# Performance work log

Hardware: AMD Instinct MI355X
Metric: run time of the kernel (lower is better)

Reference implementation:

```python
import jax, jax.numpy as jnp
import numpy as np

B, C, HID, H, W = 32, 256, 128, 32, 32  # batch, input_dim, hidden_dim, grid


def conv1x1(x, Wt, b):
    # 1x1 Conv2d == channel-mixing matmul. x: [B,Cin,H,W], Wt: [Cout,Cin]
    return jnp.einsum('oc,bchw->bohw', Wt, x) + b[None, :, None, None]


def setup_inputs() -> dict:
    key = jax.random.key(0)
    ks = jax.random.split(key, 18)
    p = lambda k, shape: (jax.random.normal(k, shape, jnp.float32) * 0.02)
    return {
        'h': jax.random.normal(ks[0], (B, C, H, W), jnp.float32),
        'm': jax.random.normal(ks[1], (B, C, H, W), jnp.float32),
        'Wq': p(ks[2], (HID, C)),  'bq': p(ks[3], (HID,)),
        'Wk': p(ks[4], (HID, C)),  'bk': p(ks[5], (HID,)),
        'Wv': p(ks[6], (C, C)),    'bv': p(ks[7], (C,)),
        'Wk2': p(ks[8], (HID, C)), 'bk2': p(ks[9], (HID,)),
        'Wv2': p(ks[10], (C, C)),  'bv2': p(ks[11], (C,)),
        'Wz': p(ks[12], (2 * C, 2 * C)), 'bz': p(ks[13], (2 * C,)),
        'Wm': p(ks[14], (3 * C, 3 * C)), 'bm': p(ks[15], (3 * C,)),
    }


def reference(h, m, Wq, bq, Wk, bk, Wv, bv, Wk2, bk2, Wv2, bv2, Wz, bz, Wm, bm):
    Bb, Cc, Hh, Ww = h.shape
    HW = Hh * Ww
    # shared query from h: [B, HID, HW]
    q = conv1x1(h, Wq, bq).reshape(Bb, -1, HW)
    # self-attention branch over h (unscaled logits, as in original)
    kh = conv1x1(h, Wk, bk).reshape(Bb, -1, HW)
    A_h = jax.nn.softmax(jnp.einsum('bdp,bdq->bpq', q, kh), axis=-1)  # [B,HW,HW]
    vh = conv1x1(h, Wv, bv).reshape(Bb, Cc, HW)
    Z_h = jnp.einsum('bpq,bcq->bcp', A_h, vh).reshape(Bb, Cc, Hh, Ww)
    # cross-attention branch over memory m with shared q
    km = conv1x1(m, Wk2, bk2).reshape(Bb, -1, HW)
    A_m = jax.nn.softmax(jnp.einsum('bdp,bdq->bpq', q, km), axis=-1)
    vm = conv1x1(m, Wv2, bv2).reshape(Bb, Cc, HW)
    Z_m = jnp.einsum('bpq,bcq->bcp', A_m, vm).reshape(Bb, Cc, Hh, Ww)
    # fuse, then LSTM-style gating
    Z = conv1x1(jnp.concatenate([Z_h, Z_m], axis=1), Wz, bz)          # [B,2C,H,W]
    comb = conv1x1(jnp.concatenate([Z, h], axis=1), Wm, bm)           # [B,3C,H,W]
    mo, mg, mi = jnp.split(comb, 3, axis=1)
    mi = jax.nn.sigmoid(mi)
    new_m = (1.0 - mi) * m + mi * jnp.tanh(mg)
    new_h = jax.nn.sigmoid(mo) * new_m
    return new_h, new_m
```

## Files before the change

kernel.cpp:

```cpp
#include <hip/hip_runtime.h>
#include <hip/hip_bf16.h>

typedef __bf16  v8bf __attribute__((ext_vector_type(8)));
typedef float   v4f  __attribute__((ext_vector_type(4)));
typedef float   f4   __attribute__((ext_vector_type(4)));
typedef unsigned short us8 __attribute__((ext_vector_type(8)));
typedef unsigned short us4 __attribute__((ext_vector_type(4)));
typedef unsigned int u32;

#define BATCH 32
#define CDIM  256
#define HW    1024

#define OFF_HBT 0L
#define OFF_MBT (OFF_HBT + 16777216L)
#define OFF_QKH (OFF_MBT + 16777216L)
#define OFF_QKM (OFF_QKH + 16777216L)
#define OFF_VH  (OFF_QKM + 8388608L)
#define OFF_VM  (OFF_VH  + 16777216L)
#define OFF_ZCT (OFF_VM  + 16777216L)
#define OFF_W   (OFF_ZCT + 33554432L)
#define OFF_B   (OFF_W   + 3866624L)
#define OFF_CMB OFF_MBT
#define WS_TOTAL (OFF_B + 2944L * 4)
#define W_QK  0
#define W_K2  65536
#define W_V   98304
#define W_V2  163840
#define W_M   491520
#define W_ZT  1081344
#define W_F   1343488
#define B_QK  0
#define B_K2  256
#define B_V   384
#define B_V2  640
#define B_F   2176

__device__ inline unsigned short f2u(float x) {
    __hip_bfloat16 h = __float2bfloat16(x);
    union { __hip_bfloat16 h; unsigned short u; } cv; cv.h = h; return cv.u;
}
__device__ inline float u2f(unsigned short u) {
    union { unsigned short u; __hip_bfloat16 h; } cv; cv.u = u; return __bfloat162float(cv.h);
}
__device__ inline float sigmoidf_(float x) {
    x = fminf(fmaxf(x, -30.f), 30.f);
    return 1.f / (1.f + __expf(-x));
}
__device__ inline float tanhf_(float x) {
    x = fminf(fmaxf(x, -15.f), 15.f);
    float e = __expf(2.f * x);
    return (e - 1.f) / (e + 1.f);
}
__device__ inline void glds16(const unsigned short* g, unsigned short* l) {
    __builtin_amdgcn_global_load_lds(
        (const __attribute__((address_space(1))) u32*)g,
        (__attribute__((address_space(3))) u32*)l, 16, 0, 0);
}

__global__ __launch_bounds__(256)
void prep(const float* __restrict__ hsrc, const float* __restrict__ msrc,
          const float* __restrict__ Wq, const float* __restrict__ Wk,
          const float* __restrict__ Wv, const float* __restrict__ Wk2,
          const float* __restrict__ Wv2, const float* __restrict__ Wz,
          const float* __restrict__ Wm,
          const float* __restrict__ bq, const float* __restrict__ bk,
          const float* __restrict__ bk2, const float* __restrict__ bv,
          const float* __restrict__ bv2, const float* __restrict__ bz,
          const float* __restrict__ bm,
          char* __restrict__ ws)
{
    __shared__ float t[64][68];
    unsigned short* wdst = (unsigned short*)(ws + OFF_W);
    float*          bdst = (float*)(ws + OFF_B);
    const int bid = blockIdx.x;
    const int tid = threadIdx.x;

    if (bid < 6025) {
        const int gid = bid * 256 + tid;
        if (gid < 1081344) {
            const float* s; int off;
            if      (gid <   32768) { s = Wq;  off = gid; }
            else if (gid <   65536) { s = Wk;  off = gid -   32768; }
            else if (gid <   98304) { s = Wk2; off = gid -   65536; }
            else if (gid <  163840) { s = Wv;  off = gid -   98304; }
            else if (gid <  229376) { s = Wv2; off = gid -  163840; }
            else if (gid <  491520) { s = Wz;  off = gid -  229376; }
            else                    { s = Wm;  off = gid -  491520; }
            wdst[gid] = f2u(s[off]);
        } else if (gid < 1343488) {
            const int idx = gid - 1081344;
            const int k = idx >> 9, j = idx & 511;
            wdst[gid] = f2u(Wz[j * 512 + k]);
        } else if (gid < 1540096) {
            const int idx = gid - 1343488;
            const int o = idx >> 8, kk = 512 + (idx & 255);
            wdst[W_F + o * 768 + kk] = f2u(Wm[o * 768 + kk]);
        } else {
            const int bi = gid - 1540096;
            if (bi < 2176) {
                const float* s; int off;
                if      (bi <  128) { s = bq;  off = bi; }
                else if (bi <  256) { s = bk;  off = bi -  128; }
                else if (bi <  384) { s = bk2; off = bi -  256; }
                else if (bi <  640) { s = bv;  off = bi -  384; }
                else if (bi <  896) { s = bv2; off = bi -  640; }
                else if (bi < 1408) { s = bz;  off = bi -  896; }
                else                { s = bm;  off = bi - 1408; }
                bdst[bi] = s[off];
            }
        }
    } else if (bid < 6028) {
        const int o = (bid - 6025) * 256 + tid;
        if (o < 768) {
            float s = bm[o];
            const float* r = Wm + (long)o * 768;
#pragma unroll 8
            for (int j = 0; j < 512; ++j) s += r[j] * bz[j];
            bdst[B_F + o] = s;
        }
    } else {
        const int tz = bid - 6028;
        const int z  = tz >> 6;
        const int p0 = (tz & 15) * 64;
        const int c0 = ((tz >> 4) & 3) * 64;
        const float* src = (z < BATCH) ? hsrc + (long)z * CDIM * HW
                                       : msrc + (long)(z - BATCH) * CDIM * HW;
        unsigned short* dst = (unsigned short*)(ws + ((z < BATCH) ? OFF_HBT : OFF_MBT))
                              + (long)((z < BATCH) ? z : z - BATCH) * HW * CDIM;
        const int r  = tid >> 4;
        const int c4 = (tid & 15) * 4;
#pragma unroll
        for (int i = 0; i < 4; ++i) {
            const f4 v = *reinterpret_cast<const f4*>(src + (long)(c0 + r + 16 * i) * HW + p0 + c4);
            t[r + 16 * i][c4 + 0] = v[0];
            t[r + 16 * i][c4 + 1] = v[1];
            t[r + 16 * i][c4 + 2] = v[2];
            t[r + 16 * i][c4 + 3] = v[3];
        }
        __syncthreads();
#pragma unroll
        for (int i = 0; i < 4; ++i) {
            const int pr = r + 16 * i;
            us4 o;
#pragma unroll
            for (int j = 0; j < 4; ++j) o[j] = f2u(t[c4 + j][pr]);
            *reinterpret_cast<us4*>(dst + (long)(p0 + pr) * CDIM + c0 + c4) = o;
        }
    }
}

__device__ __forceinline__
void gemm_core(const unsigned short* __restrict__ A, int lda,
               const unsigned short* __restrict__ A2, int lda2, int kswitch,
               const unsigned short* __restrict__ Bt, int ldb,
               unsigned short* __restrict__ Cp, int ldc,
               int K, const float* __restrict__ bias, int biasMode,
               int m0, int n0,
               unsigned short* As, unsigned short* Bs)
{
    const int tid  = threadIdx.x;
    const int lane = tid & 63;
    const int w    = tid >> 6;

    v4f acc[4][4];
#pragma unroll
    for (int i = 0; i < 4; ++i)
#pragma unroll
        for (int j = 0; j < 4; ++j) acc[i][j] = v4f{0.f, 0.f, 0.f, 0.f};

    const int wm   = (w >> 1) * 64;
    const int wn   = (w & 1) * 64;
    const int fr   = lane & 15;
    const int g    = lane >> 4;

    const int arow = (w << 3) + (lane >> 3);
    const int acol = (((lane & 7) ^ ((lane >> 3) & 7)) * 8);
    const int lbase = (w << 9);

    for (int k0 = 0; k0 < K; k0 += 64) {
        const unsigned short* Ab; int Al; int Ao;
        if (k0 < kswitch) { Ab = A;  Al = lda;  Ao = k0; }
        else              { Ab = A2; Al = lda2; Ao = k0 - kswitch; }
        const unsigned short* ga = Ab + (long)(m0 + arow) * Al + Ao + acol;
        const unsigned short* gb = Bt + (long)(n0 + arow) * ldb + k0 + acol;
#pragma unroll
        for (int i = 0; i < 4; ++i) {
            glds16(ga + (long)(32 * i) * Al, &As[i * 2048 + lbase]);
            glds16(gb + (long)(32 * i) * ldb, &Bs[i * 2048 + lbase]);
        }
        __syncthreads();
#pragma unroll
        for (int ks = 0; ks < 2; ++ks) {
            const int slot = ((ks * 4 + g) ^ (fr & 7)) * 8;
            v8bf af[4], bfv[4];
#pragma unroll
            for (int mi = 0; mi < 4; ++mi)
                af[mi] = *reinterpret_cast<const v8bf*>(&As[(wm + mi * 16 + fr) * 64 + slot]);
#pragma unroll
            for (int ni = 0; ni < 4; ++ni)
                bfv[ni] = *reinterpret_cast<const v8bf*>(&Bs[(wn + ni * 16 + fr) * 64 + slot]);
#pragma unroll
            for (int mi = 0; mi < 4; ++mi)
#pragma unroll
                for (int ni = 0; ni < 4; ++ni)
                    acc[mi][ni] = __builtin_amdgcn_mfma_f32_16x16x32_bf16(af[mi], bfv[ni], acc[mi][ni], 0, 0, 0);
        }
        __syncthreads();
    }

    const int rbase0 = m0 + wm + g * 4;
#pragma unroll
    for (int mi = 0; mi < 4; ++mi) {
#pragma unroll
        for (int ni = 0; ni < 4; ++ni) {
            const int col = n0 + wn + ni * 16 + fr;
            const int rb  = rbase0 + mi * 16;
            const float bn = (biasMode == 1) ? bias[col] : 0.f;
#pragma unroll
            for (int r = 0; r < 4; ++r) {
                float x = acc[mi][ni][r] + bn;
                if (biasMode == 2) x += bias[rb + r];
                Cp[(long)(rb + r) * ldc + col] = f2u(x);
            }
        }
    }
}

__global__ __launch_bounds__(256)
void gemm_multi(char* __restrict__ ws)
{
    __shared__ unsigned short As[128 * 64];
    __shared__ unsigned short Bs[128 * 64];
    unsigned short* wA = (unsigned short*)(ws + OFF_W);
    float*          bA = (float*)(ws + OFF_B);
    const int id = blockIdx.x;

    if (id < 512) {
        const int b = id >> 4, x = id & 7, y = (id >> 3) & 1;
        const unsigned short* A = (unsigned short*)(ws + OFF_HBT) + (long)b * 262144;
        gemm_core(A, 256, A, 256, 1 << 30, wA + W_QK, 256,
                  (unsigned short*)(ws + OFF_QKH) + (long)b * 262144, 256,
                  256, bA + B_QK, 1, x * 128, y * 128, As, Bs);
    } else if (id < 768) {
        const int idx = id - 512, b = idx >> 3, x = idx & 7;
        const unsigned short* A = (unsigned short*)(ws + OFF_MBT) + (long)b * 262144;
        gemm_core(A, 256, A, 256, 1 << 30, wA + W_K2, 256,
                  (unsigned short*)(ws + OFF_QKM) + (long)b * 131072, 128,
                  256, bA + B_K2, 1, x * 128, 0, As, Bs);
    } else if (id < 1280) {
        const int idx = id - 768, b = idx >> 4, x = idx & 1, y = (idx >> 1) & 7;
        gemm_core(wA + W_V, 256, wA + W_V, 256, 1 << 30,
                  (unsigned short*)(ws + OFF_HBT) + (long)b * 262144, 256,
                  (unsigned short*)(ws + OFF_VH) + (long)b * 262144, 1024,
                  256, bA + B_V, 2, x * 128, y * 128, As, Bs);
    } else if (id < 1792) {
        const int idx = id - 1280, b = idx >> 4, x = idx & 1, y = (idx >> 1) & 7;
        gemm_core(wA + W_V2, 256, wA + W_V2, 256, 1 << 30,
                  (unsigned short*)(ws + OFF_MBT) + (long)b * 262144, 256,
                  (unsigned short*)(ws + OFF_VM) + (long)b * 262144, 1024,
                  256, bA + B_V2, 2, x * 128, y * 128, As, Bs);
    } else {
        const int idx = id - 1792, x = idx % 6, y = idx / 6;
        gemm_core(wA + W_M, 768, wA + W_M, 768, 1 << 30, wA + W_ZT, 512,
                  wA + W_F, 768, 512, bA, 0, x * 128, y * 128, As, Bs);
    }
}

__global__ __launch_bounds__(512, 2)
void comb_gemm(const unsigned short* __restrict__ A, int lda,
               const unsigned short* __restrict__ A2, int lda2, int kswitch,
               const unsigned short* __restrict__ Bt, int ldb,
               unsigned short* __restrict__ Cp, int ldc,
               int K, const float* __restrict__ bias, int ntilesN)
{
    __shared__ unsigned short As[2][256 * 64];
    __shared__ unsigned short Bs[2][192 * 64];

    const int nwg = gridDim.x;
    const int wg  = (blockIdx.x & 7) * (nwg >> 3) + (blockIdx.x >> 3);
    const int m0  = (wg / ntilesN) * 256;
    const int n0  = (wg % ntilesN) * 192;

    const int tid  = threadIdx.x;
    const int lane = tid & 63;
    const int w    = tid >> 6;
    const int fr   = lane & 15;
    const int g    = lane >> 4;
    const int wm   = (w >> 2) * 128;
    const int wn   = (w & 3) * 48;

    const int srow   = tid >> 3;
    const int schunk = ((tid & 7) ^ (srow & 7)) * 8;
    const int sdst   = w * 512;

    v4f acc[8][3];
#pragma unroll
    for (int i = 0; i < 8; ++i)
#pragma unroll
        for (int j = 0; j < 3; ++j) acc[i][j] = v4f{0.f, 0.f, 0.f, 0.f};

    const int nt = K >> 6;

#define CSTAGE(t, bi)                                                          \
    { const int k0 = (t) * 64;                                                 \
      const unsigned short* Ab; int Al; int Ao;                                \
      if (k0 < kswitch) { Ab = A;  Al = lda;  Ao = k0; }                       \
      else              { Ab = A2; Al = lda2; Ao = k0 - kswitch; }             \
      _Pragma("unroll")                                                        \
      for (int i = 0; i < 4; ++i)                                              \
          glds16(Ab + (long)(m0 + i * 64 + srow) * Al + Ao + schunk,           \
                 &As[bi][i * 4096 + sdst]);                                    \
      _Pragma("unroll")                                                        \
      for (int i = 0; i < 3; ++i)                                              \
          glds16(Bt + (long)(n0 + i * 64 + srow) * ldb + k0 + schunk,          \
                 &Bs[bi][i * 4096 + sdst]); }

    CSTAGE(0, 0);
    CSTAGE(1, 1);

    for (int t = 0; t < nt; ++t) {
        if (t + 1 < nt) asm volatile("s_waitcnt vmcnt(7)" ::: "memory");
        else            asm volatile("s_waitcnt vmcnt(0)" ::: "memory");
        __builtin_amdgcn_s_barrier();
        asm volatile("" ::: "memory");

        const unsigned short* Ar = As[t & 1];
        const unsigned short* Br = Bs[t & 1];
        __builtin_amdgcn_s_setprio(1);
#pragma unroll
        for (int ks = 0; ks < 2; ++ks) {
            v8bf af[8], bf[3];
#pragma unroll
            for (int mi = 0; mi < 8; ++mi) {
                const int r = wm + mi * 16 + fr;
                af[mi] = *reinterpret_cast<const v8bf*>(
                    &Ar[r * 64 + ((ks * 4 + g) ^ (r & 7)) * 8]);
            }
#pragma unroll
            for (int ni = 0; ni < 3; ++ni) {
                const int r = wn + ni * 16 + fr;
                bf[ni] = *reinterpret_cast<const v8bf*>(
                    &Br[r * 64 + ((ks * 4 + g) ^ (r & 7)) * 8]);
            }
#pragma unroll
            for (int mi = 0; mi < 8; ++mi)
#pragma unroll
                for (int ni = 0; ni < 3; ++ni)
                    acc[mi][ni] = __builtin_amdgcn_mfma_f32_16x16x32_bf16(af[mi], bf[ni], acc[mi][ni], 0, 0, 0);
        }
        __builtin_amdgcn_s_setprio(0);
        asm volatile("" ::: "memory");
        __builtin_amdgcn_s_barrier();
        if (t + 2 < nt) CSTAGE(t + 2, t & 1);
    }
#undef CSTAGE

    const int rbase0 = m0 + wm + g * 4;
#pragma unroll
    for (int mi = 0; mi < 8; ++mi) {
#pragma unroll
        for (int ni = 0; ni < 3; ++ni) {
            const int col = n0 + wn + ni * 16 + fr;
            const int rb  = rbase0 + mi * 16;
            const float bn = bias[col];
#pragma unroll
            for (int r = 0; r < 4; ++r)
                Cp[(long)(rb + r) * ldc + col] = f2u(acc[mi][ni][r] + bn);
        }
    }
}

__global__ __launch_bounds__(512, 4)
void attn_fused(const unsigned short* __restrict__ Qb, long sQ, int ldq,
                const unsigned short* __restrict__ K0, long sK0, int ldk0,
                const unsigned short* __restrict__ V0,
                const unsigned short* __restrict__ K1, long sK1, int ldk1,
                const unsigned short* __restrict__ V1,
                unsigned short* __restrict__ Out, long sO)
{
    __shared__ unsigned short Ks[64 * 128];
    __shared__ unsigned short Vs[256 * 64];
    __shared__ unsigned short Ps[64 * 64];

    const int id = blockIdx.x;
    const int c8 = id & 7;
    const int k  = id >> 3;
    const int z  = c8 * 8 + (k >> 4);
    const int p0 = (k & 15) * 64;

    const int b  = (z < 32) ? z : z - 32;
    const unsigned short* Kp; const unsigned short* Vp; int ldk, outoff;
    if (z < 32) { Kp = K0 + (long)b * sK0; Vp = V0 + (long)b * 262144L; ldk = ldk0; outoff = 0; }
    else        { Kp = K1 + (long)b * sK1; Vp = V1 + (long)b * 262144L; ldk = ldk1; outoff = 256; }
    const unsigned short* Qp = Qb + (long)b * sQ;
    Out += (long)b * sO;

    const int tid  = threadIdx.x;
    const int lane = tid & 63;
    const int w    = tid >> 6;
    const int fr   = lane & 15;
    const int g    = lane >> 4;
    const int wp   = w >> 2;
    const int wq   = w & 3;

    v8bf qf[2][4];
#pragma unroll
    for (int mi = 0; mi < 2; ++mi)
#pragma unroll
        for (int ks = 0; ks < 4; ++ks)
            qf[mi][ks] = *reinterpret_cast<const v8bf*>(
                Qp + (long)(p0 + wp * 32 + mi * 16 + fr) * ldq + ks * 32 + g * 8);

    v4f vacc[2][4];
#pragma unroll
    for (int i = 0; i < 2; ++i)
#pragma unroll
        for (int j = 0; j < 4; ++j) vacc[i][j] = v4f{0.f, 0.f, 0.f, 0.f};
    float rp[2][4];
#pragma unroll
    for (int i = 0; i < 2; ++i)
#pragma unroll
        for (int r = 0; r < 4; ++r) rp[i][r] = 0.f;

    const int srow   = tid >> 4;
    const int schunk = ((tid & 15) ^ (srow & 7)) * 8;
    const int vrow   = tid >> 3;
    const int vchunk = ((tid & 7) ^ (vrow & 7)) * 8;
    const int sdst   = w * 512;
    const int kr     = wq * 16 + fr;

#define STAGE_K(t)                                                             \
    { const int kv0 = (t) * 64;                                                \
      _Pragma("unroll")                                                        \
      for (int i = 0; i < 2; ++i)                                              \
          glds16(Kp + (long)(kv0 + i * 32 + srow) * ldk + schunk,              \
                 &Ks[i * 4096 + sdst]); }
#define STAGE_V(t)                                                             \
    { const int kv0 = (t) * 64;                                                \
      _Pragma("unroll")                                                        \
      for (int i = 0; i < 4; ++i)                                              \
          glds16(Vp + (long)(i * 64 + vrow) * 1024 + kv0 + vchunk,             \
                 &Vs[i * 4096 + sdst]); }

    STAGE_K(0);

    for (int t = 0; t < 16; ++t) {
        __syncthreads();
        STAGE_V(t);

        v4f sacc[2];
#pragma unroll
        for (int mi = 0; mi < 2; ++mi) sacc[mi] = v4f{0.f, 0.f, 0.f, 0.f};
        __builtin_amdgcn_s_setprio(1);
#pragma unroll
        for (int ks = 0; ks < 4; ++ks) {
            const v8bf kf = *reinterpret_cast<const v8bf*>(
                &Ks[kr * 128 + ((ks * 4 + g) ^ (kr & 7)) * 8]);
#pragma unroll
            for (int mi = 0; mi < 2; ++mi)
                sacc[mi] = __builtin_amdgcn_mfma_f32_16x16x32_bf16(qf[mi][ks], kf, sacc[mi], 0, 0, 0);
        }
        __builtin_amdgcn_s_setprio(0);
#pragma unroll
        for (int mi = 0; mi < 2; ++mi)
#pragma unroll
            for (int r = 0; r < 4; ++r) {
                const float e = __expf(sacc[mi][r]);
                rp[mi][r] += e;
                const int prow = wp * 32 + mi * 16 + g * 4 + r;
                Ps[prow * 64 + (kr ^ ((prow & 7) << 3))] = f2u(e);
            }

        __syncthreads();
        if (t < 15) STAGE_K(t + 1);

        __builtin_amdgcn_s_setprio(1);
#pragma unroll
        for (int ks = 0; ks < 2; ++ks) {
            v8bf pf[2], vf[4];
#pragma unroll
            for (int mi = 0; mi < 2; ++mi) {
                const int pr = wp * 32 + mi * 16 + fr;
                pf[mi] = *reinterpret_cast<const v8bf*>(
                    &Ps[pr * 64 + ((ks * 4 + g) ^ (pr & 7)) * 8]);
            }
#pragma unroll
            for (int ni = 0; ni < 4; ++ni) {
                const int vr = wq * 64 + ni * 16 + fr;
                vf[ni] = *reinterpret_cast<const v8bf*>(
                    &Vs[vr * 64 + ((ks * 4 + g) ^ (vr & 7)) * 8]);
            }
#pragma unroll
            for (int mi = 0; mi < 2; ++mi)
#pragma unroll
                for (int ni = 0; ni < 4; ++ni)
                    vacc[mi][ni] = __builtin_amdgcn_mfma_f32_16x16x32_bf16(pf[mi], vf[ni], vacc[mi][ni], 0, 0, 0);
        }
        __builtin_amdgcn_s_setprio(0);
    }
#undef STAGE_K
#undef STAGE_V

    __syncthreads();
    float* red = reinterpret_cast<float*>(Ps);
#pragma unroll
    for (int mi = 0; mi < 2; ++mi)
#pragma unroll
        for (int r = 0; r < 4; ++r) {
            float v = rp[mi][r];
            v += __shfl_xor(v, 1);
            v += __shfl_xor(v, 2);
            v += __shfl_xor(v, 4);
            v += __shfl_xor(v, 8);
            if (fr == 0) red[wq * 64 + wp * 32 + mi * 16 + g * 4 + r] = v;
        }
    __syncthreads();

#pragma unroll
    for (int mi = 0; mi < 2; ++mi)
#pragma unroll
        for (int r = 0; r < 4; ++r) {
            const int pl = wp * 32 + mi * 16 + g * 4 + r;
            const float inv = 1.f / (red[pl] + red[64 + pl] + red[128 + pl] + red[192 + pl]);
#pragma unroll
            for (int ni = 0; ni < 4; ++ni)
                Out[(long)(p0 + pl) * 512 + outoff + wq * 64 + ni * 16 + fr]
                    = f2u(vacc[mi][ni][r] * inv);
        }
}

__global__ __launch_bounds__(256)
void gating(const unsigned short* __restrict__ combT, const float* __restrict__ m,
            float* __restrict__ outh, float* __restrict__ outm)
{
    const int b  = blockIdx.y;
    const int p0 = blockIdx.x * 32;
    __shared__ unsigned short t[32 * 776];
    const unsigned short* src = combT + ((long)b * HW + p0) * 768;
    const int tid = threadIdx.x;
    for (int i = tid; i < 32 * 96; i += 256) {
        const int rr = i / 96;
        const int cc = (i % 96) * 8;
        *reinterpret_cast<us8*>(&t[rr * 776 + cc]) =
            *reinterpret_cast<const us8*>(src + (long)rr * 768 + cc);
    }
    __syncthreads();
    const int pl = tid & 31;
    const int cl = tid >> 5;
    for (int ci = 0; ci < 32; ++ci) {
        const int c = ci * 8 + cl;
        const float mo = u2f(t[pl * 776 + c]);
        const float mg = u2f(t[pl * 776 + 256 + c]);
        const float mi = u2f(t[pl * 776 + 512 + c]);
        const long gi = ((long)b * CDIM + c) * HW + p0 + pl;
        const float mv = m[gi];
        const float ms = sigmoidf_(mi);
        const float nm = (1.f - ms) * mv + ms * tanhf_(mg);
        const float nh = sigmoidf_(mo) * nm;
        outh[gi] = nh;
        outm[gi] = nm;
    }
}

extern "C" void kernel_launch(void* const* d_in, const int* in_sizes, int n_in,
                              void* d_out, int out_size, void* d_ws, size_t ws_size,
                              hipStream_t stream)
{
    const float* h   = (const float*)d_in[0];
    const float* m   = (const float*)d_in[1];
    const float* Wq  = (const float*)d_in[2];
    const float* bq  = (const float*)d_in[3];
    const float* Wk  = (const float*)d_in[4];
    const float* bk  = (const float*)d_in[5];
    const float* Wv  = (const float*)d_in[6];
    const float* bv  = (const float*)d_in[7];
    const float* Wk2 = (const float*)d_in[8];
    const float* bk2 = (const float*)d_in[9];
    const float* Wv2 = (const float*)d_in[10];
    const float* bv2 = (const float*)d_in[11];
    const float* Wz  = (const float*)d_in[12];
    const float* bz  = (const float*)d_in[13];
    const float* Wm  = (const float*)d_in[14];
    const float* bm  = (const float*)d_in[15];

    char* ws = (char*)d_ws;
    if (ws_size < (size_t)WS_TOTAL) return;

    unsigned short* hT  = (unsigned short*)(ws + OFF_HBT);
    unsigned short* qkh = (unsigned short*)(ws + OFF_QKH);
    unsigned short* qkm = (unsigned short*)(ws + OFF_QKM);
    unsigned short* vh  = (unsigned short*)(ws + OFF_VH);
    unsigned short* vm  = (unsigned short*)(ws + OFF_VM);
    unsigned short* zct = (unsigned short*)(ws + OFF_ZCT);
    unsigned short* cmb = (unsigned short*)(ws + OFF_CMB);
    unsigned short* wA  = (unsigned short*)(ws + OFF_W);
    float*          bA  = (float*)(ws + OFF_B);

    float* outh = (float*)d_out;
    float* outm = outh + 8388608L;

    prep<<<dim3(10124), dim3(256), 0, stream>>>(
        h, m, Wq, Wk, Wv, Wk2, Wv2, Wz, Wm,
        bq, bk, bk2, bv, bv2, bz, bm, ws);

    gemm_multi<<<dim3(1816), dim3(256), 0, stream>>>(ws);

    attn_fused<<<dim3(1024), dim3(512), 0, stream>>>(
        qkh, 262144L, 256,
        qkh + 128, 262144L, 256, vh,
        qkm, 131072L, 128, vm,
        zct, 524288L);

    comb_gemm<<<dim3(512), dim3(512), 0, stream>>>(
        zct, 512, hT, 256, 512,
        wA + W_F, 768, cmb, 768, 768, bA + B_F, 4);

    gating<<<dim3(32, 32), dim3(256), 0, stream>>>(cmb, m, outh, outm);
}
```

Measured before the change: 240.0 us.

## Fuse LSTM gating into combine GEMM epilogue and stage Q through LDS

The combine GEMM now gives each workgroup the mo/mg/mi column slices for the same 64 channels. It applies the sigmoid/tanh gating directly from an LDS-transposed tile and writes new_h and new_m itself, which removes the separate gating kernel and the bf16 round-trip of the 768-wide comb buffer. Separately, the attention kernel loads Q into swizzled LDS via async copies instead of holding it in registers, which frees VGPRs at the cost of extra LDS reads per step.

```diff
diff --git a/kernel.cpp b/kernel.cpp
--- a/kernel.cpp
+++ b/kernel.cpp
@@ -21,7 +21,6 @@
 #define OFF_ZCT (OFF_VM  + 16777216L)
 #define OFF_W   (OFF_ZCT + 33554432L)
 #define OFF_B   (OFF_W   + 3866624L)
-#define OFF_CMB OFF_MBT
 #define WS_TOTAL (OFF_B + 2944L * 4)
 #define W_QK  0
 #define W_K2  65536
@@ -271,16 +270,16 @@
 void comb_gemm(const unsigned short* __restrict__ A, int lda,
                const unsigned short* __restrict__ A2, int lda2, int kswitch,
                const unsigned short* __restrict__ Bt, int ldb,
-               unsigned short* __restrict__ Cp, int ldc,
-               int K, const float* __restrict__ bias, int ntilesN)
+               int K, const float* __restrict__ bias,
+               const float* __restrict__ mIn,
+               float* __restrict__ outh, float* __restrict__ outm)
 {
-    __shared__ unsigned short As[2][256 * 64];
-    __shared__ unsigned short Bs[2][192 * 64];
+    __shared__ unsigned short smem[57344];
 
     const int nwg = gridDim.x;
     const int wg  = (blockIdx.x & 7) * (nwg >> 3) + (blockIdx.x >> 3);
-    const int m0  = (wg / ntilesN) * 256;
-    const int n0  = (wg % ntilesN) * 192;
+    const int m0  = (wg >> 2) * 256;
+    const int c0  = (wg & 3) * 64;
 
     const int tid  = threadIdx.x;
     const int lane = tid & 63;
@@ -304,17 +303,19 @@
 
 #define CSTAGE(t, bi)                                                          \
     { const int k0 = (t) * 64;                                                 \
+      const int ab = (bi) * 16384;                                             \
+      const int bb = 32768 + (bi) * 12288;                                     \
       const unsigned short* Ab; int Al; int Ao;                                \
       if (k0 < kswitch) { Ab = A;  Al = lda;  Ao = k0; }                       \
       else              { Ab = A2; Al = lda2; Ao = k0 - kswitch; }             \
       _Pragma("unroll")                                                        \
       for (int i = 0; i < 4; ++i)                                              \
           glds16(Ab + (long)(m0 + i * 64 + srow) * Al + Ao + schunk,           \
-                 &As[bi][i * 4096 + sdst]);                                    \
+                 &smem[ab + i * 4096 + sdst]);                                 \
       _Pragma("unroll")                                                        \
       for (int i = 0; i < 3; ++i)                                              \
-          glds16(Bt + (long)(n0 + i * 64 + srow) * ldb + k0 + schunk,          \
-                 &Bs[bi][i * 4096 + sdst]); }
+          glds16(Bt + (long)(i * 256 + c0 + srow) * ldb + k0 + schunk,         \
+                 &smem[bb + i * 4096 + sdst]); }
 
     CSTAGE(0, 0);
     CSTAGE(1, 1);
@@ -325,8 +326,8 @@
         __builtin_amdgcn_s_barrier();
         asm volatile("" ::: "memory");
 
-        const unsigned short* Ar = As[t & 1];
-        const unsigned short* Br = Bs[t & 1];
+        const unsigned short* Ar = smem + (t & 1) * 16384;
+        const unsigned short* Br = smem + 32768 + (t & 1) * 12288;
         __builtin_amdgcn_s_setprio(1);
 #pragma unroll
         for (int ks = 0; ks < 2; ++ks) {
@@ -356,18 +357,39 @@
     }
 #undef CSTAGE
 
-    const int rbase0 = m0 + wm + g * 4;
+    unsigned short* Lt = smem;
 #pragma unroll
     for (int mi = 0; mi < 8; ++mi) {
 #pragma unroll
         for (int ni = 0; ni < 3; ++ni) {
-            const int col = n0 + wn + ni * 16 + fr;
-            const int rb  = rbase0 + mi * 16;
-            const float bn = bias[col];
+            const int j  = wn + ni * 16 + fr;
+            const int cg = ((j >> 6) << 8) + c0 + (j & 63);
+            const float bn = bias[cg];
+            const int rl = wm + mi * 16 + g * 4;
 #pragma unroll
             for (int r = 0; r < 4; ++r)
-                Cp[(long)(rb + r) * ldc + col] = f2u(acc[mi][ni][r] + bn);
-        }
+                Lt[(rl + r) * 194 + j] = f2u(acc[mi][ni][r] + bn);
+        }
+    }
+    __syncthreads();
+
+    const int b     = m0 >> 10;
+    const int pbase = m0 & 1023;
+    const int pl    = tid & 255;
+    const int ch    = tid >> 8;
+#pragma unroll 4
+    for (int cc = 0; cc < 32; ++cc) {
+        const int cl = ch * 32 + cc;
+        const float mo  = u2f(Lt[pl * 194 + cl]);
+        const float mg  = u2f(Lt[pl * 194 + 64 + cl]);
+        const float mi_ = u2f(Lt[pl * 194 + 128 + cl]);
+        const long gi = ((long)(b * 256 + c0 + cl)) * 1024 + pbase + pl;
+        const float mv = mIn[gi];
+        const float ms = sigmoidf_(mi_);
+        const float nm = (1.f - ms) * mv + ms * tanhf_(mg);
+        const float nh = sigmoidf_(mo) * nm;
+        outh[gi] = nh;
+        outm[gi] = nm;
     }
 }
 
@@ -379,6 +401,7 @@
                 const unsigned short* __restrict__ V1,
                 unsigned short* __restrict__ Out, long sO)
 {
+    __shared__ unsigned short Qs[64 * 128];
     __shared__ unsigned short Ks[64 * 128];
     __shared__ unsigned short Vs[256 * 64];
     __shared__ unsigned short Ps[64 * 64];
@@ -404,14 +427,6 @@
     const int wp   = w >> 2;
     const int wq   = w & 3;
 
-    v8bf qf[2][4];
-#pragma unroll
-    for (int mi = 0; mi < 2; ++mi)
-#pragma unroll
-        for (int ks = 0; ks < 4; ++ks)
-            qf[mi][ks] = *reinterpret_cast<const v8bf*>(
-                Qp + (long)(p0 + wp * 32 + mi * 16 + fr) * ldq + ks * 32 + g * 8);
-
     v4f vacc[2][4];
 #pragma unroll
     for (int i = 0; i < 2; ++i)
@@ -430,6 +445,11 @@
     const int sdst   = w * 512;
     const int kr     = wq * 16 + fr;
 
+#define STAGE_Q()                                                              \
+    { _Pragma("unroll")                                                        \
+      for (int i = 0; i < 2; ++i)                                              \
+          glds16(Qp + (long)(p0 + i * 32 + srow) * ldq + schunk,               \
+                 &Qs[i * 4096 + sdst]); }
 #define STAGE_K(t)                                                             \
     { const int kv0 = (t) * 64;                                                \
       _Pragma("unroll")                                                        \
@@ -443,6 +463,7 @@
           glds16(Vp + (long)(i * 64 + vrow) * 1024 + kv0 + vchunk,             \
                  &Vs[i * 4096 + sdst]); }
 
+    STAGE_Q();
     STAGE_K(0);
 
     for (int t = 0; t < 16; ++t) {
@@ -458,8 +479,12 @@
             const v8bf kf = *reinterpret_cast<const v8bf*>(
                 &Ks[kr * 128 + ((ks * 4 + g) ^ (kr & 7)) * 8]);
 #pragma unroll
-            for (int mi = 0; mi < 2; ++mi)
-                sacc[mi] = __builtin_amdgcn_mfma_f32_16x16x32_bf16(qf[mi][ks], kf, sacc[mi], 0, 0, 0);
+            for (int mi = 0; mi < 2; ++mi) {
+                const int qrow = wp * 32 + mi * 16 + fr;
+                const v8bf qf = *reinterpret_cast<const v8bf*>(
+                    &Qs[qrow * 128 + ((ks * 4 + g) ^ (qrow & 7)) * 8]);
+                sacc[mi] = __builtin_amdgcn_mfma_f32_16x16x32_bf16(qf, kf, sacc[mi], 0, 0, 0);
+            }
         }
         __builtin_amdgcn_s_setprio(0);
 #pragma unroll
@@ -499,6 +524,7 @@
         }
         __builtin_amdgcn_s_setprio(0);
     }
+#undef STAGE_Q
 #undef STAGE_K
 #undef STAGE_V
 
@@ -528,39 +554,6 @@
                 Out[(long)(p0 + pl) * 512 + outoff + wq * 64 + ni * 16 + fr]
                     = f2u(vacc[mi][ni][r] * inv);
         }
-}
-
-__global__ __launch_bounds__(256)
-void gating(const unsigned short* __restrict__ combT, const float* __restrict__ m,
-            float* __restrict__ outh, float* __restrict__ outm)
-{
-    const int b  = blockIdx.y;
-    const int p0 = blockIdx.x * 32;
-    __shared__ unsigned short t[32 * 776];
-    const unsigned short* src = combT + ((long)b * HW + p0) * 768;
-    const int tid = threadIdx.x;
-    for (int i = tid; i < 32 * 96; i += 256) {
-        const int rr = i / 96;
-        const int cc = (i % 96) * 8;
-        *reinterpret_cast<us8*>(&t[rr * 776 + cc]) =
-            *reinterpret_cast<const us8*>(src + (long)rr * 768 + cc);
-    }
-    __syncthreads();
-    const int pl = tid & 31;
-    const int cl = tid >> 5;
-    for (int ci = 0; ci < 32; ++ci) {
-        const int c = ci * 8 + cl;
-        const float mo = u2f(t[pl * 776 + c]);
-        const float mg = u2f(t[pl * 776 + 256 + c]);
-        const float mi = u2f(t[pl * 776 + 512 + c]);
-        const long gi = ((long)b * CDIM + c) * HW + p0 + pl;
-        const float mv = m[gi];
-        const float ms = sigmoidf_(mi);
-        const float nm = (1.f - ms) * mv + ms * tanhf_(mg);
-        const float nh = sigmoidf_(mo) * nm;
-        outh[gi] = nh;
-        outm[gi] = nm;
-    }
 }
 
 extern "C" void kernel_launch(void* const* d_in, const int* in_sizes, int n_in,
@@ -593,7 +586,6 @@
     unsigned short* vh  = (unsigned short*)(ws + OFF_VH);
     unsigned short* vm  = (unsigned short*)(ws + OFF_VM);
     unsigned short* zct = (unsigned short*)(ws + OFF_ZCT);
-    unsigned short* cmb = (unsigned short*)(ws + OFF_CMB);
     unsigned short* wA  = (unsigned short*)(ws + OFF_W);
     float*          bA  = (float*)(ws + OFF_B);
 
@@ -614,7 +606,5 @@
 
     comb_gemm<<<dim3(512), dim3(512), 0, stream>>>(
         zct, 512, hT, 256, 512,
-        wA + W_F, 768, cmb, 768, 768, bA + B_F, 4);
-
-    gating<<<dim3(32, 32), dim3(256), 0, stream>>>(cmb, m, outh, outm);
-}
+        wA + W_F, 768, 768, bA + B_F, m, outh, outm);
+}
```

Measured after the change: 207.4 us. 13.6% less time.
